# Kernel tuning notes

Measured on AMD Instinct MI355X. Metric: run time of the kernel, lower is better.

The kernel has to match this reference:

```python
import jax, jax.numpy as jnp
import numpy as np

N_NODES = 10000
IN_CH = 128
OUT_CH = 128
N_EDGES = 320000


def setup_inputs() -> dict:
    key = jax.random.key(0)
    k1, k2, k3, k4 = jax.random.split(key, 4)
    x = jax.random.normal(k1, (N_NODES, IN_CH), dtype=jnp.float32)
    edge_index = jax.random.randint(k2, (N_EDGES, 2), 0, N_NODES, dtype=jnp.int64)
    # Linear weights (torch stores [out, in]); scale like kaiming-uniform-ish
    w = jax.random.normal(k3, (OUT_CH, IN_CH), dtype=jnp.float32) / np.sqrt(IN_CH)
    b = jax.random.normal(k4, (OUT_CH, IN_CH), dtype=jnp.float32) / np.sqrt(IN_CH)
    return {"x": x, "edge_index": edge_index, "w": w, "b": b}


def reference(x, edge_index, w, b):
    n = x.shape[0]
    # Each edge (i, j) contributes x[j] to node i and x[i] to node j (undirected).
    src = jnp.concatenate([edge_index[:, 1], edge_index[:, 0]])  # feature source
    dst = jnp.concatenate([edge_index[:, 0], edge_index[:, 1]])  # aggregation target
    # segment-sum of gathered neighbor features -> [n, in_ch]
    agg_sum = jax.ops.segment_sum(x[src], dst, num_segments=n)
    deg = jax.ops.segment_sum(jnp.ones_like(dst, dtype=x.dtype), dst, num_segments=n)
    # mean with zero fallback for isolated nodes (original uses zeros vector)
    agg = jnp.where(deg[:, None] > 0, agg_sum / jnp.maximum(deg, 1.0)[:, None], 0.0)
    # out = ReLU(agg @ w^T + x @ b^T)
    return jax.nn.relu(agg @ w.T + x @ b.T)
```

## Files before the change

### kernel.cpp

```cpp
#include <hip/hip_runtime.h>

#define N_NODES 10000
#define CH 128
#define N_EDGES 320000
#define CAP 128
#define CSTR 16
#define NPB 16


__device__ __forceinline__ unsigned short f2bf(float f) {
    unsigned u = __float_as_uint(f);
    return (unsigned short)((u + 0x7FFFu + ((u >> 16) & 1u)) >> 16);
}
__device__ __forceinline__ float bf2f(unsigned short h) {
    return __uint_as_float(((unsigned)h) << 16);
}

__global__ __launch_bounds__(256) void fill_convert_kernel(
    const int* __restrict__ ei,
    const float* __restrict__ x,
    int* __restrict__ cursor,
    unsigned short* __restrict__ adj,
    unsigned short* __restrict__ xb)
{
    const int t = blockIdx.x * blockDim.x + threadIdx.x;

    const float4 c0 = ((const float4*)x)[2 * t];
    const float4 c1 = ((const float4*)x)[2 * t + 1];
    ushort4 o0, o1;
    o0.x = f2bf(c0.x); o0.y = f2bf(c0.y); o0.z = f2bf(c0.z); o0.w = f2bf(c0.w);
    o1.x = f2bf(c1.x); o1.y = f2bf(c1.y); o1.z = f2bf(c1.z); o1.w = f2bf(c1.w);
    ((ushort4*)xb)[2 * t]     = o0;
    ((ushort4*)xb)[2 * t + 1] = o1;

    const int4 p = ((const int4*)ei)[t];
    const bool v0 = (unsigned)p.x < N_NODES && (unsigned)p.y < N_NODES;
    const bool v1 = (unsigned)p.z < N_NODES && (unsigned)p.w < N_NODES;
    int s0 = 0, s1 = 0, s2 = 0, s3 = 0;
    if (v0) { s0 = atomicAdd(&cursor[p.x * CSTR], 1); s1 = atomicAdd(&cursor[p.y * CSTR], 1); }
    if (v1) { s2 = atomicAdd(&cursor[p.z * CSTR], 1); s3 = atomicAdd(&cursor[p.w * CSTR], 1); }
    if (v0) {
        if (s0 < CAP) adj[(size_t)p.x * CAP + s0] = (unsigned short)p.y;
        if (s1 < CAP) adj[(size_t)p.y * CAP + s1] = (unsigned short)p.x;
    }
    if (v1) {
        if (s2 < CAP) adj[(size_t)p.z * CAP + s2] = (unsigned short)p.w;
        if (s3 < CAP) adj[(size_t)p.w * CAP + s3] = (unsigned short)p.z;
    }
}

__global__ __launch_bounds__(256) void gather_gemm_kernel(
    const float* __restrict__ x,
    const unsigned short* __restrict__ xb,
    const int* __restrict__ cursor,
    const unsigned short* __restrict__ adj,
    const float* __restrict__ w,
    const float* __restrict__ b,
    float* __restrict__ out)
{
    __shared__ float sh_a[NPB * CH];
    __shared__ float sh_x[NPB * CH];
    const int tid   = threadIdx.x;
    const int node0 = blockIdx.x * NPB;

    ((float4*)sh_x)[tid]       = ((const float4*)(x + (size_t)node0 * CH))[tid];
    ((float4*)sh_x)[tid + 256] = ((const float4*)(x + (size_t)node0 * CH))[tid + 256];

    {
        const int wv   = tid >> 6;
        const int lane = tid & 63;
        const int h    = lane >> 5;
        const int l    = lane & 31;
#pragma unroll
        for (int q = 0; q < 4; ++q) {
            const int ln   = wv + 4 * q;
            const int node = node0 + ln;
            const int deg  = cursor[node * CSTR];
            const int d    = deg < CAP ? deg : CAP;
            const unsigned short* nb = adj + (size_t)node * CAP;

            float4 acc = {0.f, 0.f, 0.f, 0.f};
            const int nit = (d + 1) >> 1;
#pragma unroll 4
            for (int it = 0; it < nit; ++it) {
                const int idx = 2 * it + h;
                int j = nb[idx];
                j = j < N_NODES ? j : 0;
                const ushort4 u = ((const ushort4*)(xb + (size_t)j * CH))[l];
                const float m = idx < d ? 1.0f : 0.0f;
                acc.x += m * bf2f(u.x);
                acc.y += m * bf2f(u.y);
                acc.z += m * bf2f(u.z);
                acc.w += m * bf2f(u.w);
            }
            acc.x += __shfl_xor(acc.x, 32, 64);
            acc.y += __shfl_xor(acc.y, 32, 64);
            acc.z += __shfl_xor(acc.z, 32, 64);
            acc.w += __shfl_xor(acc.w, 32, 64);
            if (h == 0) {
                const float inv = deg > 0 ? 1.0f / (float)deg : 0.0f;
                float4 o4;
                o4.x = acc.x * inv; o4.y = acc.y * inv;
                o4.z = acc.z * inv; o4.w = acc.w * inv;
                ((float4*)(sh_a + (size_t)ln * CH))[l] = o4;
            }
        }
    }
    __syncthreads();

    const int o = tid & 127;
    const int g = tid >> 7;
    const float4* wr = (const float4*)(w + (size_t)o * CH);
    const float4* br = (const float4*)(b + (size_t)o * CH);
    const float4* A  = (const float4*)(sh_a + (size_t)(g * 8) * CH);
    const float4* X  = (const float4*)(sh_x + (size_t)(g * 8) * CH);

    float acc[8] = {0.f, 0.f, 0.f, 0.f, 0.f, 0.f, 0.f, 0.f};
#pragma unroll 4
    for (int k = 0; k < CH / 4; ++k) {
        const float4 wv4 = wr[k];
        const float4 bv4 = br[k];
#pragma unroll
        for (int n = 0; n < 8; ++n) {
            const float4 a4 = A[n * (CH / 4) + k];
            const float4 x4 = X[n * (CH / 4) + k];
            acc[n] += a4.x * wv4.x + a4.y * wv4.y + a4.z * wv4.z + a4.w * wv4.w
                    + x4.x * bv4.x + x4.y * bv4.y + x4.z * bv4.z + x4.w * bv4.w;
        }
    }
#pragma unroll
    for (int n = 0; n < 8; ++n) {
        const int node = node0 + g * 8 + n;
        const float v = acc[n];
        out[(size_t)node * CH + o] = v > 0.f ? v : 0.f;
    }
}

extern "C" void kernel_launch(void* const* d_in, const int* in_sizes, int n_in,
                              void* d_out, int out_size, void* d_ws, size_t ws_size,
                              hipStream_t stream)
{
    const float* x  = (const float*)d_in[0];
    const int*   ei = (const int*)d_in[1];
    const float* w  = (const float*)d_in[2];
    const float* b  = (const float*)d_in[3];
    float*       out = (float*)d_out;

    int*            cursor = (int*)d_ws;
    unsigned short* adj    = (unsigned short*)((char*)d_ws + 640000);
    unsigned short* xb     = (unsigned short*)((char*)d_ws + 3200000);

    hipMemsetAsync(d_ws, 0, (size_t)N_NODES * CSTR * sizeof(int), stream);

    fill_convert_kernel<<<625, 256, 0, stream>>>(ei, x, cursor, adj, xb);
    gather_gemm_kernel<<<625, 256, 0, stream>>>(x, xb, cursor, adj, w, b, out);
}
```

Measured before the change: 143.3 us.

## Replace global adjacency build with per-block edge scan into shared-memory buckets

Drops the global cursor/adjacency build, its memset and the global atomics. Each of 250 blocks now scans the entire edge list and uses LDS atomics to bucket the neighbours of its own 40 nodes, then does the gather and the GEMM in the same kernel. The goal is to remove contended global atomics and the adjacency round trip through memory. The cost is that every block re-reads the whole edge list, which multiplies edge traffic by the block count, and only 250 blocks are launched.

```diff
diff --git a/kernel.cpp b/kernel.cpp
--- a/kernel.cpp
+++ b/kernel.cpp
@@ -4,8 +4,9 @@
 #define CH 128
 #define N_EDGES 320000
 #define CAP 128
-#define CSTR 16
-#define NPB 16
+#define NPB 40
+#define NBLK 250
+#define TPB 512
 
 
 __device__ __forceinline__ unsigned short f2bf(float f) {
@@ -16,15 +17,10 @@
     return __uint_as_float(((unsigned)h) << 16);
 }
 
-__global__ __launch_bounds__(256) void fill_convert_kernel(
-    const int* __restrict__ ei,
-    const float* __restrict__ x,
-    int* __restrict__ cursor,
-    unsigned short* __restrict__ adj,
-    unsigned short* __restrict__ xb)
+__global__ __launch_bounds__(256) void convert_kernel(const float* __restrict__ x,
+                                                      unsigned short* __restrict__ xb)
 {
     const int t = blockIdx.x * blockDim.x + threadIdx.x;
-
     const float4 c0 = ((const float4*)x)[2 * t];
     const float4 c1 = ((const float4*)x)[2 * t + 1];
     ushort4 o0, o1;
@@ -32,39 +28,52 @@
     o1.x = f2bf(c1.x); o1.y = f2bf(c1.y); o1.z = f2bf(c1.z); o1.w = f2bf(c1.w);
     ((ushort4*)xb)[2 * t]     = o0;
     ((ushort4*)xb)[2 * t + 1] = o1;
-
-    const int4 p = ((const int4*)ei)[t];
-    const bool v0 = (unsigned)p.x < N_NODES && (unsigned)p.y < N_NODES;
-    const bool v1 = (unsigned)p.z < N_NODES && (unsigned)p.w < N_NODES;
-    int s0 = 0, s1 = 0, s2 = 0, s3 = 0;
-    if (v0) { s0 = atomicAdd(&cursor[p.x * CSTR], 1); s1 = atomicAdd(&cursor[p.y * CSTR], 1); }
-    if (v1) { s2 = atomicAdd(&cursor[p.z * CSTR], 1); s3 = atomicAdd(&cursor[p.w * CSTR], 1); }
-    if (v0) {
-        if (s0 < CAP) adj[(size_t)p.x * CAP + s0] = (unsigned short)p.y;
-        if (s1 < CAP) adj[(size_t)p.y * CAP + s1] = (unsigned short)p.x;
-    }
-    if (v1) {
-        if (s2 < CAP) adj[(size_t)p.z * CAP + s2] = (unsigned short)p.w;
-        if (s3 < CAP) adj[(size_t)p.w * CAP + s3] = (unsigned short)p.z;
-    }
 }
 
-__global__ __launch_bounds__(256) void gather_gemm_kernel(
+__global__ __launch_bounds__(TPB) void mega_kernel(
     const float* __restrict__ x,
     const unsigned short* __restrict__ xb,
-    const int* __restrict__ cursor,
-    const unsigned short* __restrict__ adj,
+    const int* __restrict__ ei,
     const float* __restrict__ w,
     const float* __restrict__ b,
     float* __restrict__ out)
 {
-    __shared__ float sh_a[NPB * CH];
-    __shared__ float sh_x[NPB * CH];
-    const int tid   = threadIdx.x;
-    const int node0 = blockIdx.x * NPB;
+    __shared__ unsigned short bucket[NPB][CAP];
+    __shared__ int   cnt[NPB];
+    __shared__ float sh_a[NPB][CH];
+    __shared__ float sh_x[NPB][CH];
 
-    ((float4*)sh_x)[tid]       = ((const float4*)(x + (size_t)node0 * CH))[tid];
-    ((float4*)sh_x)[tid + 256] = ((const float4*)(x + (size_t)node0 * CH))[tid + 256];
+    const int tid = threadIdx.x;
+    const int lo  = blockIdx.x * NPB;
+
+    if (tid < NPB) cnt[tid] = 0;
+    __syncthreads();
+
+    const int4* e4 = (const int4*)ei;
+    for (int t = tid; t < N_EDGES / 2; t += TPB) {
+        const int4 p = e4[t];
+        {   const unsigned r = (unsigned)(p.x - lo);
+            if (r < NPB) { const int s = atomicAdd(&cnt[r], 1);
+                           if (s < CAP) bucket[r][s] = (unsigned short)p.y; } }
+        {   const unsigned r = (unsigned)(p.y - lo);
+            if (r < NPB) { const int s = atomicAdd(&cnt[r], 1);
+                           if (s < CAP) bucket[r][s] = (unsigned short)p.x; } }
+        {   const unsigned r = (unsigned)(p.z - lo);
+            if (r < NPB) { const int s = atomicAdd(&cnt[r], 1);
+                           if (s < CAP) bucket[r][s] = (unsigned short)p.w; } }
+        {   const unsigned r = (unsigned)(p.w - lo);
+            if (r < NPB) { const int s = atomicAdd(&cnt[r], 1);
+                           if (s < CAP) bucket[r][s] = (unsigned short)p.z; } }
+    }
+
+    {
+        const float4* xs = (const float4*)(x + (size_t)lo * CH);
+        float4* sx = (float4*)sh_x;
+        sx[tid] = xs[tid];
+        sx[tid + TPB] = xs[tid + TPB];
+        if (tid < NPB * CH / 4 - 2 * TPB) sx[tid + 2 * TPB] = xs[tid + 2 * TPB];
+    }
+    __syncthreads();
 
     {
         const int wv   = tid >> 6;
@@ -72,19 +81,17 @@
         const int h    = lane >> 5;
         const int l    = lane & 31;
 #pragma unroll
-        for (int q = 0; q < 4; ++q) {
-            const int ln   = wv + 4 * q;
-            const int node = node0 + ln;
-            const int deg  = cursor[node * CSTR];
-            const int d    = deg < CAP ? deg : CAP;
-            const unsigned short* nb = adj + (size_t)node * CAP;
+        for (int q = 0; q < 5; ++q) {
+            const int ln  = wv + 8 * q;
+            const int deg = cnt[ln];
+            const int d   = deg < CAP ? deg : CAP;
 
             float4 acc = {0.f, 0.f, 0.f, 0.f};
             const int nit = (d + 1) >> 1;
 #pragma unroll 4
             for (int it = 0; it < nit; ++it) {
                 const int idx = 2 * it + h;
-                int j = nb[idx];
+                int j = bucket[ln][idx];
                 j = j < N_NODES ? j : 0;
                 const ushort4 u = ((const ushort4*)(xb + (size_t)j * CH))[l];
                 const float m = idx < d ? 1.0f : 0.0f;
@@ -102,37 +109,39 @@
                 float4 o4;
                 o4.x = acc.x * inv; o4.y = acc.y * inv;
                 o4.z = acc.z * inv; o4.w = acc.w * inv;
-                ((float4*)(sh_a + (size_t)ln * CH))[l] = o4;
+                ((float4*)sh_a[ln])[l] = o4;
             }
         }
     }
     __syncthreads();
 
-    const int o = tid & 127;
-    const int g = tid >> 7;
-    const float4* wr = (const float4*)(w + (size_t)o * CH);
-    const float4* br = (const float4*)(b + (size_t)o * CH);
-    const float4* A  = (const float4*)(sh_a + (size_t)(g * 8) * CH);
-    const float4* X  = (const float4*)(sh_x + (size_t)(g * 8) * CH);
+    {
+        const int o = tid & 127;
+        const int g = tid >> 7;
+        const float4* wr = (const float4*)(w + (size_t)o * CH);
+        const float4* br = (const float4*)(b + (size_t)o * CH);
 
-    float acc[8] = {0.f, 0.f, 0.f, 0.f, 0.f, 0.f, 0.f, 0.f};
-#pragma unroll 4
-    for (int k = 0; k < CH / 4; ++k) {
-        const float4 wv4 = wr[k];
-        const float4 bv4 = br[k];
+        float acc[10];
 #pragma unroll
-        for (int n = 0; n < 8; ++n) {
-            const float4 a4 = A[n * (CH / 4) + k];
-            const float4 x4 = X[n * (CH / 4) + k];
-            acc[n] += a4.x * wv4.x + a4.y * wv4.y + a4.z * wv4.z + a4.w * wv4.w
-                    + x4.x * bv4.x + x4.y * bv4.y + x4.z * bv4.z + x4.w * bv4.w;
+        for (int n = 0; n < 10; ++n) acc[n] = 0.f;
+
+        for (int k = 0; k < CH / 4; ++k) {
+            const float4 wv4 = wr[k];
+            const float4 bv4 = br[k];
+#pragma unroll
+            for (int n = 0; n < 10; ++n) {
+                const float4 a4 = ((const float4*)sh_a[g * 10 + n])[k];
+                const float4 x4 = ((const float4*)sh_x[g * 10 + n])[k];
+                acc[n] += a4.x * wv4.x + a4.y * wv4.y + a4.z * wv4.z + a4.w * wv4.w
+                        + x4.x * bv4.x + x4.y * bv4.y + x4.z * bv4.z + x4.w * bv4.w;
+            }
         }
-    }
 #pragma unroll
-    for (int n = 0; n < 8; ++n) {
-        const int node = node0 + g * 8 + n;
-        const float v = acc[n];
-        out[(size_t)node * CH + o] = v > 0.f ? v : 0.f;
+        for (int n = 0; n < 10; ++n) {
+            const int node = lo + g * 10 + n;
+            const float v = acc[n];
+            out[(size_t)node * CH + o] = v > 0.f ? v : 0.f;
+        }
     }
 }
 
@@ -146,12 +155,8 @@
     const float* b  = (const float*)d_in[3];
     float*       out = (float*)d_out;
 
-    int*            cursor = (int*)d_ws;
-    unsigned short* adj    = (unsigned short*)((char*)d_ws + 640000);
-    unsigned short* xb     = (unsigned short*)((char*)d_ws + 3200000);
+    unsigned short* xb = (unsigned short*)d_ws;
 
-    hipMemsetAsync(d_ws, 0, (size_t)N_NODES * CSTR * sizeof(int), stream);
-
-    fill_convert_kernel<<<625, 256, 0, stream>>>(ei, x, cursor, adj, xb);
-    gather_gemm_kernel<<<625, 256, 0, stream>>>(x, xb, cursor, adj, w, b, out);
+    convert_kernel<<<625, 256, 0, stream>>>(x, xb);
+    mega_kernel<<<NBLK, TPB, 0, stream>>>(x, xb, ei, w, b, out);
 }
```

New measurement: 215.7 us. 50.6% more time.

## Halve nodes per block, pack degree counters densely, retile gather-GEMM to 2x2

Applied to the files above, without the earlier changes.

The degree-counter array loses its 16-int padding stride and becomes a dense int array, which shrinks the memset and the workspace offsets. The gather-GEMM kernel now handles 8 nodes per block instead of 16 across 1250 blocks, so each wave gathers 2 nodes instead of 4. The GEMM phase becomes a 2-node by 2-output-channel register tile per thread. The aim is more blocks for better latency hiding and a smaller memset, at the cost of more atomic contention on shared cache lines and each block re-reading the w and b matrices for fewer nodes.

```diff
diff --git a/kernel.cpp b/kernel.cpp
--- a/kernel.cpp
+++ b/kernel.cpp
@@ -4,8 +4,8 @@
 #define CH 128
 #define N_EDGES 320000
 #define CAP 128
-#define CSTR 16
-#define NPB 16
+#define NPB 8
+#define GG_BLOCKS 1250
 
 
 __device__ __forceinline__ unsigned short f2bf(float f) {
@@ -37,8 +37,8 @@
     const bool v0 = (unsigned)p.x < N_NODES && (unsigned)p.y < N_NODES;
     const bool v1 = (unsigned)p.z < N_NODES && (unsigned)p.w < N_NODES;
     int s0 = 0, s1 = 0, s2 = 0, s3 = 0;
-    if (v0) { s0 = atomicAdd(&cursor[p.x * CSTR], 1); s1 = atomicAdd(&cursor[p.y * CSTR], 1); }
-    if (v1) { s2 = atomicAdd(&cursor[p.z * CSTR], 1); s3 = atomicAdd(&cursor[p.w * CSTR], 1); }
+    if (v0) { s0 = atomicAdd(&cursor[p.x], 1); s1 = atomicAdd(&cursor[p.y], 1); }
+    if (v1) { s2 = atomicAdd(&cursor[p.z], 1); s3 = atomicAdd(&cursor[p.w], 1); }
     if (v0) {
         if (s0 < CAP) adj[(size_t)p.x * CAP + s0] = (unsigned short)p.y;
         if (s1 < CAP) adj[(size_t)p.y * CAP + s1] = (unsigned short)p.x;
@@ -58,13 +58,12 @@
     const float* __restrict__ b,
     float* __restrict__ out)
 {
-    __shared__ float sh_a[NPB * CH];
-    __shared__ float sh_x[NPB * CH];
+    __shared__ float sh_a[NPB][CH];
+    __shared__ float sh_x[NPB][CH];
     const int tid   = threadIdx.x;
     const int node0 = blockIdx.x * NPB;
 
-    ((float4*)sh_x)[tid]       = ((const float4*)(x + (size_t)node0 * CH))[tid];
-    ((float4*)sh_x)[tid + 256] = ((const float4*)(x + (size_t)node0 * CH))[tid + 256];
+    ((float4*)sh_x)[tid] = ((const float4*)(x + (size_t)node0 * CH))[tid];
 
     {
         const int wv   = tid >> 6;
@@ -72,10 +71,10 @@
         const int h    = lane >> 5;
         const int l    = lane & 31;
 #pragma unroll
-        for (int q = 0; q < 4; ++q) {
-            const int ln   = wv + 4 * q;
+        for (int q = 0; q < 2; ++q) {
+            const int ln   = 2 * wv + q;
             const int node = node0 + ln;
-            const int deg  = cursor[node * CSTR];
+            const int deg  = cursor[node];
             const int d    = deg < CAP ? deg : CAP;
             const unsigned short* nb = adj + (size_t)node * CAP;
 
@@ -102,37 +101,46 @@
                 float4 o4;
                 o4.x = acc.x * inv; o4.y = acc.y * inv;
                 o4.z = acc.z * inv; o4.w = acc.w * inv;
-                ((float4*)(sh_a + (size_t)ln * CH))[l] = o4;
+                ((float4*)sh_a[ln])[l] = o4;
             }
         }
     }
     __syncthreads();
 
-    const int o = tid & 127;
-    const int g = tid >> 7;
-    const float4* wr = (const float4*)(w + (size_t)o * CH);
-    const float4* br = (const float4*)(b + (size_t)o * CH);
-    const float4* A  = (const float4*)(sh_a + (size_t)(g * 8) * CH);
-    const float4* X  = (const float4*)(sh_x + (size_t)(g * 8) * CH);
+    {
+        const int c  = tid & 63;
+        const int ng = tid >> 6;
+        const int n0 = 2 * ng, n1 = 2 * ng + 1;
 
-    float acc[8] = {0.f, 0.f, 0.f, 0.f, 0.f, 0.f, 0.f, 0.f};
-#pragma unroll 4
-    for (int k = 0; k < CH / 4; ++k) {
-        const float4 wv4 = wr[k];
-        const float4 bv4 = br[k];
-#pragma unroll
-        for (int n = 0; n < 8; ++n) {
-            const float4 a4 = A[n * (CH / 4) + k];
-            const float4 x4 = X[n * (CH / 4) + k];
-            acc[n] += a4.x * wv4.x + a4.y * wv4.y + a4.z * wv4.z + a4.w * wv4.w
-                    + x4.x * bv4.x + x4.y * bv4.y + x4.z * bv4.z + x4.w * bv4.w;
+        const float4* A0 = (const float4*)sh_a[n0];
+        const float4* A1 = (const float4*)sh_a[n1];
+        const float4* X0 = (const float4*)sh_x[n0];
+        const float4* X1 = (const float4*)sh_x[n1];
+        const float4* w0 = (const float4*)(w + (size_t)c * CH);
+        const float4* w1 = (const float4*)(w + (size_t)(c + 64) * CH);
+        const float4* b0 = (const float4*)(b + (size_t)c * CH);
+        const float4* b1 = (const float4*)(b + (size_t)(c + 64) * CH);
+
+        float a00 = 0.f, a01 = 0.f, a10 = 0.f, a11 = 0.f;
+#pragma unroll 2
+        for (int k = 0; k < CH / 4; ++k) {
+            const float4 wv0 = w0[k], wv1 = w1[k];
+            const float4 bv0 = b0[k], bv1 = b1[k];
+            const float4 q0 = A0[k], q1 = A1[k];
+            const float4 y0 = X0[k], y1 = X1[k];
+            a00 += q0.x * wv0.x + q0.y * wv0.y + q0.z * wv0.z + q0.w * wv0.w
+                 + y0.x * bv0.x + y0.y * bv0.y + y0.z * bv0.z + y0.w * bv0.w;
+            a01 += q0.x * wv1.x + q0.y * wv1.y + q0.z * wv1.z + q0.w * wv1.w
+                 + y0.x * bv1.x + y0.y * bv1.y + y0.z * bv1.z + y0.w * bv1.w;
+            a10 += q1.x * wv0.x + q1.y * wv0.y + q1.z * wv0.z + q1.w * wv0.w
+                 + y1.x * bv0.x + y1.y * bv0.y + y1.z * bv0.z + y1.w * bv0.w;
+            a11 += q1.x * wv1.x + q1.y * wv1.y + q1.z * wv1.z + q1.w * wv1.w
+                 + y1.x * bv1.x + y1.y * bv1.y + y1.z * bv1.z + y1.w * bv1.w;
         }
-    }
-#pragma unroll
-    for (int n = 0; n < 8; ++n) {
-        const int node = node0 + g * 8 + n;
-        const float v = acc[n];
-        out[(size_t)node * CH + o] = v > 0.f ? v : 0.f;
+        out[(size_t)(node0 + n0) * CH + c]      = a00 > 0.f ? a00 : 0.f;
+        out[(size_t)(node0 + n0) * CH + c + 64] = a01 > 0.f ? a01 : 0.f;
+        out[(size_t)(node0 + n1) * CH + c]      = a10 > 0.f ? a10 : 0.f;
+        out[(size_t)(node0 + n1) * CH + c + 64] = a11 > 0.f ? a11 : 0.f;
     }
 }
 
@@ -147,11 +155,11 @@
     float*       out = (float*)d_out;
 
     int*            cursor = (int*)d_ws;
-    unsigned short* adj    = (unsigned short*)((char*)d_ws + 640000);
-    unsigned short* xb     = (unsigned short*)((char*)d_ws + 3200000);
+    unsigned short* adj    = (unsigned short*)((char*)d_ws + 40000);
+    unsigned short* xb     = (unsigned short*)((char*)d_ws + 2600000);
 
-    hipMemsetAsync(d_ws, 0, (size_t)N_NODES * CSTR * sizeof(int), stream);
+    hipMemsetAsync(d_ws, 0, N_NODES * sizeof(int), stream);
 
     fill_convert_kernel<<<625, 256, 0, stream>>>(ei, x, cursor, adj, xb);
-    gather_gemm_kernel<<<625, 256, 0, stream>>>(x, xb, cursor, adj, w, b, out);
+    gather_gemm_kernel<<<GG_BLOCKS, 256, 0, stream>>>(x, xb, cursor, adj, w, b, out);
 }
```

Result: slower. 203.3 us (+41.9%).
